# Kernel tuning notes

Measured on AMD Instinct MI355X. Metric: run time of the kernel, lower is better.

## Reference

```python
import jax, jax.numpy as jnp
import numpy as np

D = 1024      # input_dim
H = 16        # num_heads
DH = D // H   # head dim
HID = 4 * D   # SwiGLU hidden
WIN = 128
B, S = 2, 1024


def setup_inputs() -> dict:
    key = jax.random.key(0)
    ks = jax.random.split(key, 16)
    n = lambda k, sh, sc=0.02: jax.random.normal(k, sh, dtype=jnp.float32) * sc
    inp = {
        "fusion": jax.random.normal(ks[0], (B, S, D), dtype=jnp.float32),
        "visual": jax.random.normal(ks[1], (B, S, D), dtype=jnp.float32),
        "text": jax.random.normal(ks[2], (B, S, D), dtype=jnp.float32),
        "audio": jax.random.normal(ks[3], (B, S, D), dtype=jnp.float32),
        "ln1_g": jnp.ones((D,), jnp.float32),
        "ln1_b": jnp.zeros((D,), jnp.float32),
        "Wqkv": n(ks[4], (D, 3 * D)),
        "bqkv": jnp.zeros((3 * D,), jnp.float32),
        "Wo": n(ks[5], (D, D)),
        "bo": jnp.zeros((D,), jnp.float32),
        "ln2_g": jnp.ones((D,), jnp.float32),
        "ln2_b": jnp.zeros((D,), jnp.float32),
        "W1": n(ks[6], (D, HID)),
        "b1": jnp.zeros((HID,), jnp.float32),
        "W2": n(ks[7], (D, HID)),
        "b2": jnp.zeros((HID,), jnp.float32),
        "W3": n(ks[8], (HID, D)),
        "b3": jnp.zeros((D,), jnp.float32),
    }
    return inp


def _layernorm(x, g, b, eps=1e-5):
    mu = jnp.mean(x, axis=-1, keepdims=True)
    var = jnp.var(x, axis=-1, keepdims=True)
    return (x - mu) * jax.lax.rsqrt(var + eps) * g + b


def _block(x, ln1_g, ln1_b, Wqkv, bqkv, Wo, bo, ln2_g, ln2_b, W1, b1, W2, b2, W3, b3):
    # x: [N, S, D] (N = 4*B streams stacked)
    N, S_, _ = x.shape
    h = _layernorm(x, ln1_g, ln1_b)
    qkv = h @ Wqkv + bqkv                              # [N, S, 3D]
    q, k, v = jnp.split(qkv, 3, axis=-1)
    to_heads = lambda t: t.reshape(N, S_, H, DH).transpose(0, 2, 1, 3)  # [N,H,S,DH]
    q, k, v = to_heads(q), to_heads(k), to_heads(v)
    scores = jnp.einsum("nhqd,nhkd->nhqk", q, k) / np.sqrt(DH)
    i = jnp.arange(S_)
    band = jnp.abs(i[:, None] - i[None, :]) <= WIN     # [S, S] local window mask
    scores = jnp.where(band, scores, -jnp.inf)
    probs = jax.nn.softmax(scores, axis=-1)
    ctx = jnp.einsum("nhqk,nhkd->nhqd", probs, v)      # [N,H,S,DH]
    ctx = ctx.transpose(0, 2, 1, 3).reshape(N, S_, D)
    x = x + (ctx @ Wo + bo)
    h2 = _layernorm(x, ln2_g, ln2_b)
    ffn = (jax.nn.silu(h2 @ W1 + b1) * (h2 @ W2 + b2)) @ W3 + b3
    return x + ffn


def reference(fusion, visual, text, audio, ln1_g, ln1_b, Wqkv, bqkv, Wo, bo,
              ln2_g, ln2_b, W1, b1, W2, b2, W3, b3):
    # Same layer applied to each modality -> stack and run once.
    x = jnp.concatenate([fusion, visual, text, audio], axis=0)  # [4B, S, D]
    y = _block(x, ln1_g, ln1_b, Wqkv, bqkv, Wo, bo, ln2_g, ln2_b,
               W1, b1, W2, b2, W3, b3)
    f, vi, t, a = jnp.split(y, 4, axis=0)
    return (f, vi, t, a)
```

## Files before the change

### kernel.cpp

```cpp
#include <hip/hip_runtime.h>

#define S_LEN  1024
#define DMODEL 1024
#define NHEAD  16
#define DHEAD  64
#define MROWS  8192
#define HIDDIM 4096
#define WINR   128

typedef __attribute__((ext_vector_type(8))) short bf16x8;
typedef __attribute__((ext_vector_type(4))) float f32x4;

__device__ __forceinline__ float bf2f(unsigned short u){ return __uint_as_float(((unsigned)u) << 16); }
__device__ __forceinline__ unsigned short f2bf(float f){
  unsigned u = __float_as_uint(f);
  u += 0x7FFFu + ((u >> 16) & 1u);
  return (unsigned short)(u >> 16);
}

__device__ __forceinline__ void gload_lds16(const unsigned short* g, unsigned short* l){
  __builtin_amdgcn_global_load_lds((const __attribute__((address_space(1))) unsigned int*)g,
                                   (__attribute__((address_space(3))) unsigned int*)l, 16, 0, 0);
}

__global__ __launch_bounds__(256) void transpose_w(const float* __restrict__ in,
                                                   unsigned short* __restrict__ out,
                                                   int R, int C){
  __shared__ float tile[32][33];
  const int c0 = blockIdx.x * 32;
  const int r0 = blockIdx.y * 32;
  const int tx = threadIdx.x & 31;
  const int ty = threadIdx.x >> 5;
  #pragma unroll
  for (int i = 0; i < 32; i += 8)
    tile[ty + i][tx] = in[(size_t)(r0 + ty + i) * C + c0 + tx];
  __syncthreads();
  #pragma unroll
  for (int i = 0; i < 32; i += 8)
    out[(size_t)(c0 + ty + i) * R + r0 + tx] = f2bf(tile[tx][ty + i]);
}

__global__ __launch_bounds__(256) void ln_kernel(const float* __restrict__ s0, const float* __restrict__ s1,
                                                 const float* __restrict__ s2, const float* __restrict__ s3,
                                                 const float* __restrict__ g, const float* __restrict__ b,
                                                 unsigned short* __restrict__ out){
  const int row = blockIdx.x;
  const int t = threadIdx.x;
  const float* src = (row < 2048) ? s0 : (row < 4096) ? s1 : (row < 6144) ? s2 : s3;
  const float* x = src + (size_t)(row & 2047) * DMODEL;
  float4 v = *(const float4*)&x[t * 4];
  float sum  = v.x + v.y + v.z + v.w;
  float ssum = v.x*v.x + v.y*v.y + v.z*v.z + v.w*v.w;
  #pragma unroll
  for (int o = 32; o > 0; o >>= 1){
    sum  += __shfl_down(sum, o);
    ssum += __shfl_down(ssum, o);
  }
  __shared__ float red[8];
  if ((t & 63) == 0){ red[t >> 6] = sum; red[4 + (t >> 6)] = ssum; }
  __syncthreads();
  sum  = red[0] + red[1] + red[2] + red[3];
  ssum = red[4] + red[5] + red[6] + red[7];
  const float mu  = sum * (1.f / DMODEL);
  const float var = ssum * (1.f / DMODEL) - mu * mu;
  const float rs  = rsqrtf(var + 1e-5f);
  float4 gg = *(const float4*)&g[t * 4];
  float4 bb = *(const float4*)&b[t * 4];
  ushort4 o;
  o.x = f2bf((v.x - mu) * rs * gg.x + bb.x);
  o.y = f2bf((v.y - mu) * rs * gg.y + bb.y);
  o.z = f2bf((v.z - mu) * rs * gg.z + bb.z);
  o.w = f2bf((v.w - mu) * rs * gg.w + bb.w);
  *(ushort4*)&out[(size_t)row * DMODEL + t * 4] = o;
}

__global__ __launch_bounds__(256) void attn_kernel(const unsigned short* __restrict__ qh,
                                                   const unsigned short* __restrict__ kh,
                                                   const unsigned short* __restrict__ vt,
                                                   unsigned short* __restrict__ ctx){
  __shared__ unsigned short Ks[64 * 64];
  __shared__ unsigned short Vs[64 * 64];
  __shared__ unsigned short Ps[4][16 * 64];
  const int bx = blockIdx.x;
  const int qt = bx & 15, hd = (bx >> 4) & 15, n = bx >> 8;
  const int q0 = qt * 64;
  const int tid = threadIdx.x, lane = tid & 63, w = tid >> 6;
  const int hi = lane >> 4, lo = lane & 15;
  const size_t headoff = (size_t)(n * NHEAD + hd) * S_LEN * DHEAD;
  const unsigned short* kb = kh + headoff;
  const unsigned short* vb = vt + headoff;

  const int qg = q0 + w * 16 + lo;
  bf16x8 bq0 = *(const bf16x8*)(qh + headoff + (size_t)qg * DHEAD + hi * 8);
  bf16x8 bq1 = *(const bf16x8*)(qh + headoff + (size_t)qg * DHEAD + 32 + hi * 8);

  f32x4 oa[4];
  const f32x4 zero = {0.f, 0.f, 0.f, 0.f};
  #pragma unroll
  for (int dj = 0; dj < 4; dj++) oa[dj] = zero;
  float m = -20.f, lsum = 0.f;

  int t_first = q0 - WINR; if (t_first < 0) t_first = 0;
  int t_last  = q0 + 63 + WINR; if (t_last > S_LEN - 1) t_last = S_LEN - 1;

  const int sk = ((lane & 7) ^ (lane >> 3)) * 8;
  const int px = (lo & 7) * 8;

  for (int tb = t_first; tb <= t_last; tb += 64){
    __syncthreads();
    #pragma unroll
    for (int p = 0; p < 2; p++){
      const int r = w * 16 + p * 8 + (lane >> 3);
      gload_lds16(kb + (size_t)(tb + r) * DHEAD + sk, Ks + (w * 16 + p * 8) * 64);
      gload_lds16(vb + (size_t)r * S_LEN + tb + sk, Vs + (w * 16 + p * 8) * 64);
    }
    __syncthreads();

    f32x4 sc[4];
    #pragma unroll
    for (int j = 0; j < 4; j++){
      const int row = j * 16 + lo;
      bf16x8 ak0 = *(const bf16x8*)&Ks[row * 64 + ((hi * 8) ^ px)];
      bf16x8 ak1 = *(const bf16x8*)&Ks[row * 64 + ((32 + hi * 8) ^ px)];
      sc[j] = __builtin_amdgcn_mfma_f32_16x16x32_bf16(ak0, bq0, zero, 0, 0, 0);
      sc[j] = __builtin_amdgcn_mfma_f32_16x16x32_bf16(ak1, bq1, sc[j], 0, 0, 0);
    }

    float mloc = -1e30f;
    #pragma unroll
    for (int j = 0; j < 4; j++)
      #pragma unroll
      for (int r = 0; r < 4; r++){
        const int key = tb + j * 16 + hi * 4 + r;
        float s = sc[j][r] * 0.125f;
        s = ((unsigned)(key - qg + WINR) <= 2u * WINR) ? s : -1e9f;
        sc[j][r] = s;
        mloc = fmaxf(mloc, s);
      }
    mloc = fmaxf(mloc, __shfl_xor(mloc, 16));
    mloc = fmaxf(mloc, __shfl_xor(mloc, 32));
    const float nm = fmaxf(m, mloc);
    const float scale = __expf(m - nm);
    m = nm;
    float psum = 0.f;
    #pragma unroll
    for (int j = 0; j < 4; j++){
      float p0 = __expf(sc[j][0] - nm), p1 = __expf(sc[j][1] - nm);
      float p2 = __expf(sc[j][2] - nm), p3 = __expf(sc[j][3] - nm);
      psum += (p0 + p1) + (p2 + p3);
      ushort4 pw = { f2bf(p0), f2bf(p1), f2bf(p2), f2bf(p3) };
      *(ushort4*)&Ps[w][lo * 64 + ((hi * 4 + 16 * j) ^ px)] = pw;
    }
    psum += __shfl_xor(psum, 16);
    psum += __shfl_xor(psum, 32);
    lsum = lsum * scale + psum;

    float scr[4];
    #pragma unroll
    for (int r = 0; r < 4; r++) scr[r] = __shfl(scale, (lane & 48) + hi * 4 + r);
    #pragma unroll
    for (int dj = 0; dj < 4; dj++)
      #pragma unroll
      for (int r = 0; r < 4; r++) oa[dj][r] *= scr[r];

    bf16x8 pa0 = *(const bf16x8*)&Ps[w][lo * 64 + ((hi * 8) ^ px)];
    bf16x8 pa1 = *(const bf16x8*)&Ps[w][lo * 64 + ((32 + hi * 8) ^ px)];
    #pragma unroll
    for (int dj = 0; dj < 4; dj++){
      const int dr = dj * 16 + lo;
      bf16x8 bv0 = *(const bf16x8*)&Vs[dr * 64 + ((hi * 8) ^ px)];
      bf16x8 bv1 = *(const bf16x8*)&Vs[dr * 64 + ((32 + hi * 8) ^ px)];
      oa[dj] = __builtin_amdgcn_mfma_f32_16x16x32_bf16(pa0, bv0, oa[dj], 0, 0, 0);
      oa[dj] = __builtin_amdgcn_mfma_f32_16x16x32_bf16(pa1, bv1, oa[dj], 0, 0, 0);
    }
  }

  const float inv = 1.f / lsum;
  float invr[4];
  #pragma unroll
  for (int r = 0; r < 4; r++) invr[r] = __shfl(inv, (lane & 48) + hi * 4 + r);
  #pragma unroll
  for (int dj = 0; dj < 4; dj++)
    #pragma unroll
    for (int r = 0; r < 4; r++){
      const int srow = q0 + w * 16 + hi * 4 + r;
      ctx[((size_t)(n * S_LEN + srow)) * DMODEL + hd * DHEAD + dj * 16 + lo] =
          f2bf(oa[dj][r] * invr[r]);
    }
}

struct GemmP {
  const unsigned short* A;
  const unsigned short* Bt;
  int K;
  int N;
  const float* bias;
  const float* r0; const float* r1; const float* r2; const float* r3;
  unsigned short* oq; unsigned short* ok; unsigned short* ov;
  float* of;
};

template<int MODE>
__global__ __launch_bounds__(512, 2) void gemm_bn128(GemmP p){
  __shared__ unsigned short ldsA[2][256 * 64];
  __shared__ unsigned short ldsB[2][128 * 64];
  const int tid  = threadIdx.x;
  const int lane = tid & 63;
  const int w    = tid >> 6;
  const int lo   = lane & 15, hi = lane >> 4;
  const int l3   = lane >> 3;
  const int sk   = ((lane & 7) ^ l3) * 8;
  const int wm   = (w >> 1) * 64;
  const int wn   = (w & 1) * 64;
  const int K    = p.K;

  const int nwg = gridDim.x;
  const int cpx = nwg >> 3;
  const int bsw = ((int)blockIdx.x & 7) * cpx + ((int)blockIdx.x >> 3);
  const int ntn = p.N >> 7;
  const int m0  = (bsw / ntn) * 256;
  const int n0  = (bsw % ntn) * 128;

  f32x4 acc[4][4];
  const f32x4 zero = {0.f, 0.f, 0.f, 0.f};
  #pragma unroll
  for (int i = 0; i < 4; i++)
    #pragma unroll
    for (int j = 0; j < 4; j++) acc[i][j] = zero;

  auto STAGE = [&](int T){
    const int cur = T & 1;
    const int kb  = T * 64;
    #pragma unroll
    for (int i = 0; i < 4; i++){
      const int r0 = w * 32 + i * 8;
      gload_lds16(p.A + (size_t)(m0 + r0 + l3) * K + kb + sk, &ldsA[cur][r0 * 64]);
    }
    #pragma unroll
    for (int i = 0; i < 2; i++){
      const int r0 = w * 16 + i * 8;
      gload_lds16(p.Bt + (size_t)(n0 + r0 + l3) * K + kb + sk, &ldsB[cur][r0 * 64]);
    }
  };

  STAGE(0);

  const int NT = K >> 6;
  for (int T = 0; T < NT; T++){
    const int cur = T & 1;
    if (T + 1 < NT){
      STAGE(T + 1);
      asm volatile("s_waitcnt vmcnt(6)" ::: "memory");
    } else {
      asm volatile("s_waitcnt vmcnt(0)" ::: "memory");
    }
    __builtin_amdgcn_sched_barrier(0);
    __builtin_amdgcn_s_barrier();
    const unsigned short* As_ = ldsA[cur];
    const unsigned short* Bs_ = ldsB[cur];
    #pragma unroll
    for (int kk = 0; kk < 2; kk++){
      bf16x8 af[4], bfr[4];
      #pragma unroll
      for (int i = 0; i < 4; i++){
        const int R = wm + i * 16 + lo;
        af[i] = *(const bf16x8*)&As_[R * 64 + (((kk * 4 + hi) ^ (R & 7)) * 8)];
      }
      #pragma unroll
      for (int j = 0; j < 4; j++){
        const int R = wn + j * 16 + lo;
        bfr[j] = *(const bf16x8*)&Bs_[R * 64 + (((kk * 4 + hi) ^ (R & 7)) * 8)];
      }
      #pragma unroll
      for (int i = 0; i < 4; i++)
        #pragma unroll
        for (int j = 0; j < 4; j++)
          acc[i][j] = __builtin_amdgcn_mfma_f32_16x16x32_bf16(bfr[j], af[i], acc[i][j], 0, 0, 0);
    }
    __builtin_amdgcn_s_barrier();
  }

  if constexpr (MODE == 1 || MODE == 4){
    const float* rs = p.r0;
    if constexpr (MODE == 1){
      const int rblk = m0 + wm;
      rs = (rblk < 2048) ? p.r0 : (rblk < 4096) ? p.r1 : (rblk < 6144) ? p.r2 : p.r3;
    }
    #pragma unroll
    for (int i = 0; i < 4; i++){
      const int row = m0 + wm + i * 16 + lo;
      #pragma unroll
      for (int j = 0; j < 4; j++){
        const int cb = n0 + wn + j * 16 + hi * 4;
        float4 b4 = *(const float4*)&p.bias[cb];
        float4 r4;
        if constexpr (MODE == 1) r4 = *(const float4*)&rs[(size_t)(row & 2047) * DMODEL + cb];
        else                     r4 = *(const float4*)&rs[(size_t)row * DMODEL + cb];
        float4 v;
        v.x = acc[i][j][0] + b4.x + r4.x;
        v.y = acc[i][j][1] + b4.y + r4.y;
        v.z = acc[i][j][2] + b4.z + r4.z;
        v.w = acc[i][j][3] + b4.w + r4.w;
        *(float4*)&p.of[(size_t)row * DMODEL + cb] = v;
      }
    }
  } else {
    __syncthreads();
    unsigned short* sl = &ldsA[0][0] + w * 4096;
    const int nseq = (m0 + wm) >> 10;
    const int sof  = (m0 + wm) & 1023;
    const bool isV = (n0 >> 10) == 2;
    if (!isV){
      #pragma unroll
      for (int i = 0; i < 4; i++){
        const int row = i * 16 + lo;
        #pragma unroll
        for (int j = 0; j < 4; j++){
          const int c  = j * 16 + hi * 4;
          const int cb = n0 + wn + c;
          float4 b4 = *(const float4*)&p.bias[cb];
          ushort4 o = { f2bf(acc[i][j][0] + b4.x), f2bf(acc[i][j][1] + b4.y),
                        f2bf(acc[i][j][2] + b4.z), f2bf(acc[i][j][3] + b4.w) };
          *(ushort4*)&sl[row * 64 + (((c >> 3) ^ (row & 7)) * 8) + (c & 7)] = o;
        }
      }
      asm volatile("s_waitcnt lgkmcnt(0)" ::: "memory");
      __builtin_amdgcn_sched_barrier(0);
      #pragma unroll
      for (int rep = 0; rep < 8; rep++){
        const int row = rep * 8 + l3;
        const int ch  = lane & 7;
        bf16x8 val = *(const bf16x8*)&sl[row * 64 + ((ch ^ (row & 7)) * 8)];
        const int cg = n0 + wn + ch * 8;
        const int hh = (cg & 1023) >> 6, d0 = cg & 63;
        unsigned short* dst = (cg >> 10) ? p.ok : p.oq;
        *(bf16x8*)&dst[((size_t)((nseq * NHEAD + hh) * S_LEN) + sof + row) * DHEAD + d0] = val;
      }
    } else {
      #pragma unroll
      for (int i = 0; i < 4; i++){
        const int s = i * 16 + lo;
        #pragma unroll
        for (int j = 0; j < 4; j++){
          const int cb = n0 + wn + j * 16 + hi * 4;
          float4 b4 = *(const float4*)&p.bias[cb];
          #pragma unroll
          for (int r = 0; r < 4; r++){
            const int d = j * 16 + hi * 4 + r;
            const float bv = (r == 0) ? b4.x : (r == 1) ? b4.y : (r == 2) ? b4.z : b4.w;
            sl[d * 64 + (((s >> 3) ^ (d & 7)) * 8) + (s & 7)] = f2bf(acc[i][j][r] + bv);
          }
        }
      }
      asm volatile("s_waitcnt lgkmcnt(0)" ::: "memory");
      __builtin_amdgcn_sched_barrier(0);
      #pragma unroll
      for (int rep = 0; rep < 8; rep++){
        const int d  = rep * 8 + l3;
        const int ch = lane & 7;
        bf16x8 val = *(const bf16x8*)&sl[d * 64 + ((ch ^ (d & 7)) * 8)];
        const int cg = n0 + wn + d;
        const int hh = (cg & 1023) >> 6, dd = cg & 63;
        *(bf16x8*)&p.ov[((size_t)((nseq * NHEAD + hh) * DHEAD) + dd) * S_LEN + sof + ch * 8] = val;
      }
    }
  }
}

__global__ __launch_bounds__(512, 2) void gemm_ffn(const unsigned short* __restrict__ A,
                                                   const unsigned short* __restrict__ B1t,
                                                   const unsigned short* __restrict__ B2t,
                                                   const float* __restrict__ b1,
                                                   const float* __restrict__ b2,
                                                   unsigned short* __restrict__ out){
  __shared__ unsigned short ldsA[2][256 * 64];
  __shared__ unsigned short ldsB[2][2][128 * 64];
  const int tid  = threadIdx.x;
  const int lane = tid & 63;
  const int w    = tid >> 6;
  const int lo   = lane & 15, hi = lane >> 4;
  const int l3   = lane >> 3;
  const int sk   = ((lane & 7) ^ l3) * 8;
  const int wm   = (w >> 1) * 64;
  const int wn   = (w & 1) * 64;
  const int K    = DMODEL;

  const int nwg = gridDim.x;
  const int cpx = nwg >> 3;
  const int bsw = ((int)blockIdx.x & 7) * cpx + ((int)blockIdx.x >> 3);
  const int m0  = (bsw >> 5) * 256;
  const int n0  = (bsw & 31) * 128;

  f32x4 a1[4][4], a2[4][4];
  const f32x4 zero = {0.f, 0.f, 0.f, 0.f};
  #pragma unroll
  for (int i = 0; i < 4; i++)
    #pragma unroll
    for (int j = 0; j < 4; j++){ a1[i][j] = zero; a2[i][j] = zero; }

  auto STAGE = [&](int T){
    const int cur = T & 1;
    const int kb  = T * 64;
    #pragma unroll
    for (int i = 0; i < 4; i++){
      const int r0 = w * 32 + i * 8;
      gload_lds16(A + (size_t)(m0 + r0 + l3) * K + kb + sk, &ldsA[cur][r0 * 64]);
    }
    #pragma unroll
    for (int i = 0; i < 2; i++){
      const int r0 = w * 16 + i * 8;
      gload_lds16(B1t + (size_t)(n0 + r0 + l3) * K + kb + sk, &ldsB[cur][0][r0 * 64]);
      gload_lds16(B2t + (size_t)(n0 + r0 + l3) * K + kb + sk, &ldsB[cur][1][r0 * 64]);
    }
  };

  STAGE(0);

  const int NT = K >> 6;
  for (int T = 0; T < NT; T++){
    const int cur = T & 1;
    if (T + 1 < NT){
      STAGE(T + 1);
      asm volatile("s_waitcnt vmcnt(8)" ::: "memory");
    } else {
      asm volatile("s_waitcnt vmcnt(0)" ::: "memory");
    }
    __builtin_amdgcn_sched_barrier(0);
    __builtin_amdgcn_s_barrier();
    const unsigned short* As_  = ldsA[cur];
    const unsigned short* Bs1_ = ldsB[cur][0];
    const unsigned short* Bs2_ = ldsB[cur][1];
    #pragma unroll
    for (int kk = 0; kk < 2; kk++){
      bf16x8 af[4], bf1[4], bf2[4];
      #pragma unroll
      for (int i = 0; i < 4; i++){
        const int R = wm + i * 16 + lo;
        af[i] = *(const bf16x8*)&As_[R * 64 + (((kk * 4 + hi) ^ (R & 7)) * 8)];
      }
      #pragma unroll
      for (int j = 0; j < 4; j++){
        const int R = wn + j * 16 + lo;
        const int off = R * 64 + (((kk * 4 + hi) ^ (R & 7)) * 8);
        bf1[j] = *(const bf16x8*)&Bs1_[off];
        bf2[j] = *(const bf16x8*)&Bs2_[off];
      }
      #pragma unroll
      for (int i = 0; i < 4; i++)
        #pragma unroll
        for (int j = 0; j < 4; j++){
          a1[i][j] = __builtin_amdgcn_mfma_f32_16x16x32_bf16(bf1[j], af[i], a1[i][j], 0, 0, 0);
          a2[i][j] = __builtin_amdgcn_mfma_f32_16x16x32_bf16(bf2[j], af[i], a2[i][j], 0, 0, 0);
        }
    }
    __builtin_amdgcn_s_barrier();
  }

  __syncthreads();
  unsigned short* sl = &ldsA[0][0] + w * 4096;
  #pragma unroll
  for (int i = 0; i < 4; i++){
    const int row = i * 16 + lo;
    #pragma unroll
    for (int j = 0; j < 4; j++){
      const int c  = j * 16 + hi * 4;
      const int cb = n0 + wn + c;
      float4 g1 = *(const float4*)&b1[cb];
      float4 g2 = *(const float4*)&b2[cb];
      float v1[4] = { a1[i][j][0] + g1.x, a1[i][j][1] + g1.y, a1[i][j][2] + g1.z, a1[i][j][3] + g1.w };
      float v2[4] = { a2[i][j][0] + g2.x, a2[i][j][1] + g2.y, a2[i][j][2] + g2.z, a2[i][j][3] + g2.w };
      ushort4 o;
      o.x = f2bf(v1[0] / (1.f + __expf(-v1[0])) * v2[0]);
      o.y = f2bf(v1[1] / (1.f + __expf(-v1[1])) * v2[1]);
      o.z = f2bf(v1[2] / (1.f + __expf(-v1[2])) * v2[2]);
      o.w = f2bf(v1[3] / (1.f + __expf(-v1[3])) * v2[3]);
      *(ushort4*)&sl[row * 64 + (((c >> 3) ^ (row & 7)) * 8) + (c & 7)] = o;
    }
  }
  asm volatile("s_waitcnt lgkmcnt(0)" ::: "memory");
  __builtin_amdgcn_sched_barrier(0);
  #pragma unroll
  for (int rep = 0; rep < 8; rep++){
    const int row = rep * 8 + l3;
    const int ch  = lane & 7;
    bf16x8 val = *(const bf16x8*)&sl[row * 64 + ((ch ^ (row & 7)) * 8)];
    *(bf16x8*)&out[(size_t)(m0 + wm + row) * HIDDIM + n0 + wn + ch * 8] = val;
  }
}

extern "C" void kernel_launch(void* const* d_in, const int* in_sizes, int n_in,
                              void* d_out, int out_size, void* d_ws, size_t ws_size,
                              hipStream_t stream){
  const float* fin  = (const float*)d_in[0];
  const float* vis  = (const float*)d_in[1];
  const float* txt  = (const float*)d_in[2];
  const float* aud  = (const float*)d_in[3];
  const float* ln1g = (const float*)d_in[4];
  const float* ln1b = (const float*)d_in[5];
  const float* Wqkv = (const float*)d_in[6];
  const float* bqkv = (const float*)d_in[7];
  const float* Wo   = (const float*)d_in[8];
  const float* bo   = (const float*)d_in[9];
  const float* ln2g = (const float*)d_in[10];
  const float* ln2b = (const float*)d_in[11];
  const float* W1   = (const float*)d_in[12];
  const float* b1   = (const float*)d_in[13];
  const float* W2   = (const float*)d_in[14];
  const float* b2   = (const float*)d_in[15];
  const float* W3   = (const float*)d_in[16];
  const float* b3   = (const float*)d_in[17];

  char* ws = (char*)d_ws;
  unsigned short* Wqkv_t = (unsigned short*)(ws + 0);
  unsigned short* Wo_t   = (unsigned short*)(ws + 6291456);
  unsigned short* W1t    = (unsigned short*)(ws + 8388608);
  unsigned short* W2t    = (unsigned short*)(ws + 16777216);
  unsigned short* W3t    = (unsigned short*)(ws + 25165824);
  unsigned short* h      = (unsigned short*)(ws + 33554432);
  unsigned short* qh     = (unsigned short*)(ws + 50331648);
  unsigned short* kh     = (unsigned short*)(ws + 67108864);
  unsigned short* vhT    = (unsigned short*)(ws + 83886080);
  unsigned short* ctx    = (unsigned short*)(ws + 100663296);
  float*          x1     = (float*)(ws + 117440512);
  unsigned short* t1     = qh;

  transpose_w<<<dim3(3072/32, 1024/32), 256, 0, stream>>>(Wqkv, Wqkv_t, 1024, 3072);
  transpose_w<<<dim3(1024/32, 1024/32), 256, 0, stream>>>(Wo,   Wo_t,   1024, 1024);
  transpose_w<<<dim3(4096/32, 1024/32), 256, 0, stream>>>(W1,   W1t,    1024, 4096);
  transpose_w<<<dim3(4096/32, 1024/32), 256, 0, stream>>>(W2,   W2t,    1024, 4096);
  transpose_w<<<dim3(1024/32, 4096/32), 256, 0, stream>>>(W3,   W3t,    4096, 1024);

  ln_kernel<<<MROWS, 256, 0, stream>>>(fin, vis, txt, aud, ln1g, ln1b, h);

  {
    GemmP p{};
    p.A = h; p.Bt = Wqkv_t; p.K = 1024; p.N = 3072; p.bias = bqkv;
    p.oq = qh; p.ok = kh; p.ov = vhT;
    gemm_bn128<0><<<768, 512, 0, stream>>>(p);
  }

  attn_kernel<<<2048, 256, 0, stream>>>(qh, kh, vhT, ctx);

  {
    GemmP p{};
    p.A = ctx; p.Bt = Wo_t; p.K = 1024; p.N = 1024; p.bias = bo;
    p.r0 = fin; p.r1 = vis; p.r2 = txt; p.r3 = aud;
    p.of = x1;
    gemm_bn128<1><<<256, 512, 0, stream>>>(p);
  }

  ln_kernel<<<MROWS, 256, 0, stream>>>(x1, x1 + (size_t)2048 * 1024, x1 + (size_t)4096 * 1024,
                                       x1 + (size_t)6144 * 1024, ln2g, ln2b, h);

  gemm_ffn<<<1024, 512, 0, stream>>>(h, W1t, W2t, b1, b2, t1);

  {
    GemmP p{};
    p.A = t1; p.Bt = W3t; p.K = HIDDIM; p.N = 1024; p.bias = b3;
    p.r0 = x1;
    p.of = (float*)d_out;
    gemm_bn128<4><<<256, 512, 0, stream>>>(p);
  }

  (void)in_sizes; (void)n_in; (void)out_size; (void)ws_size;
}
```

Measured before the change: 402.9 us.

## Split FFN gate/up GEMM into two phases with staggered A/B prefetch

Restructures the dual-B SwiGLU GEMM main loop into two half-phases: the first computes the W1 product while prefetching the next A tile, and the second computes the W2 product while prefetching the next B1/B2 tiles. Loads are issued after the barrier, with finer-grained vmcnt waits, so global-to-LDS traffic overlaps MFMA work more evenly. It also uses s_setprio around the MFMA blocks and fewer live B fragments to cut register pressure. The cost is an extra barrier per K step and A fragments being re-read from LDS twice.

```diff
diff --git a/kernel.cpp b/kernel.cpp
--- a/kernel.cpp
+++ b/kernel.cpp
@@ -374,7 +374,8 @@
                                                    const float* __restrict__ b2,
                                                    unsigned short* __restrict__ out){
   __shared__ unsigned short ldsA[2][256 * 64];
-  __shared__ unsigned short ldsB[2][2][128 * 64];
+  __shared__ unsigned short ldsB1[2][128 * 64];
+  __shared__ unsigned short ldsB2[2][128 * 64];
   const int tid  = threadIdx.x;
   const int lane = tid & 63;
   const int w    = tid >> 6;
@@ -383,7 +384,6 @@
   const int sk   = ((lane & 7) ^ l3) * 8;
   const int wm   = (w >> 1) * 64;
   const int wn   = (w & 1) * 64;
-  const int K    = DMODEL;
 
   const int nwg = gridDim.x;
   const int cpx = nwg >> 3;
@@ -398,41 +398,48 @@
     #pragma unroll
     for (int j = 0; j < 4; j++){ a1[i][j] = zero; a2[i][j] = zero; }
 
-  auto STAGE = [&](int T){
+  auto STAGE_A = [&](int T){
     const int cur = T & 1;
     const int kb  = T * 64;
     #pragma unroll
-    for (int i = 0; i < 4; i++){
-      const int r0 = w * 32 + i * 8;
-      gload_lds16(A + (size_t)(m0 + r0 + l3) * K + kb + sk, &ldsA[cur][r0 * 64]);
-    }
-    #pragma unroll
-    for (int i = 0; i < 2; i++){
-      const int r0 = w * 16 + i * 8;
-      gload_lds16(B1t + (size_t)(n0 + r0 + l3) * K + kb + sk, &ldsB[cur][0][r0 * 64]);
-      gload_lds16(B2t + (size_t)(n0 + r0 + l3) * K + kb + sk, &ldsB[cur][1][r0 * 64]);
+    for (int c = 0; c < 4; c++){
+      const int r0 = c * 64 + w * 8;
+      gload_lds16(A + (size_t)(m0 + r0 + l3) * DMODEL + kb + sk, &ldsA[cur][r0 * 64]);
     }
   };
-
-  STAGE(0);
-
-  const int NT = K >> 6;
+  auto STAGE_B = [&](int T){
+    const int cur = T & 1;
+    const int kb  = T * 64;
+    #pragma unroll
+    for (int h = 0; h < 2; h++){
+      const int r0 = h * 64 + w * 8;
+      gload_lds16(B1t + (size_t)(n0 + r0 + l3) * DMODEL + kb + sk, &ldsB1[cur][r0 * 64]);
+    }
+    #pragma unroll
+    for (int h = 0; h < 2; h++){
+      const int r0 = h * 64 + w * 8;
+      gload_lds16(B2t + (size_t)(n0 + r0 + l3) * DMODEL + kb + sk, &ldsB2[cur][r0 * 64]);
+    }
+  };
+
+  STAGE_A(0);
+  STAGE_B(0);
+
+  const int NT = DMODEL >> 6;
   for (int T = 0; T < NT; T++){
     const int cur = T & 1;
-    if (T + 1 < NT){
-      STAGE(T + 1);
-      asm volatile("s_waitcnt vmcnt(8)" ::: "memory");
-    } else {
-      asm volatile("s_waitcnt vmcnt(0)" ::: "memory");
-    }
+    const unsigned short* As_  = ldsA[cur];
+    const unsigned short* Bs1_ = ldsB1[cur];
+    const unsigned short* Bs2_ = ldsB2[cur];
+
+    asm volatile("s_waitcnt vmcnt(2)" ::: "memory");
     __builtin_amdgcn_sched_barrier(0);
     __builtin_amdgcn_s_barrier();
-    const unsigned short* As_  = ldsA[cur];
-    const unsigned short* Bs1_ = ldsB[cur][0];
-    const unsigned short* Bs2_ = ldsB[cur][1];
+
+    if (T + 1 < NT) STAGE_A(T + 1);
     #pragma unroll
     for (int kk = 0; kk < 2; kk++){
-      bf16x8 af[4], bf1[4], bf2[4];
+      bf16x8 af[4], bfr[4];
       #pragma unroll
       for (int i = 0; i < 4; i++){
         const int R = wm + i * 16 + lo;
@@ -441,19 +448,44 @@
       #pragma unroll
       for (int j = 0; j < 4; j++){
         const int R = wn + j * 16 + lo;
-        const int off = R * 64 + (((kk * 4 + hi) ^ (R & 7)) * 8);
-        bf1[j] = *(const bf16x8*)&Bs1_[off];
-        bf2[j] = *(const bf16x8*)&Bs2_[off];
-      }
+        bfr[j] = *(const bf16x8*)&Bs1_[R * 64 + (((kk * 4 + hi) ^ (R & 7)) * 8)];
+      }
+      __builtin_amdgcn_s_setprio(1);
       #pragma unroll
       for (int i = 0; i < 4; i++)
         #pragma unroll
-        for (int j = 0; j < 4; j++){
-          a1[i][j] = __builtin_amdgcn_mfma_f32_16x16x32_bf16(bf1[j], af[i], a1[i][j], 0, 0, 0);
-          a2[i][j] = __builtin_amdgcn_mfma_f32_16x16x32_bf16(bf2[j], af[i], a2[i][j], 0, 0, 0);
-        }
-    }
+        for (int j = 0; j < 4; j++)
+          a1[i][j] = __builtin_amdgcn_mfma_f32_16x16x32_bf16(bfr[j], af[i], a1[i][j], 0, 0, 0);
+      __builtin_amdgcn_s_setprio(0);
+    }
+
+    if (T + 1 < NT) asm volatile("s_waitcnt vmcnt(4)" ::: "memory");
+    else            asm volatile("s_waitcnt vmcnt(0)" ::: "memory");
+    __builtin_amdgcn_sched_barrier(0);
     __builtin_amdgcn_s_barrier();
+
+    if (T + 1 < NT) STAGE_B(T + 1);
+    #pragma unroll
+    for (int kk = 0; kk < 2; kk++){
+      bf16x8 af[4], bfr[4];
+      #pragma unroll
+      for (int i = 0; i < 4; i++){
+        const int R = wm + i * 16 + lo;
+        af[i] = *(const bf16x8*)&As_[R * 64 + (((kk * 4 + hi) ^ (R & 7)) * 8)];
+      }
+      #pragma unroll
+      for (int j = 0; j < 4; j++){
+        const int R = wn + j * 16 + lo;
+        bfr[j] = *(const bf16x8*)&Bs2_[R * 64 + (((kk * 4 + hi) ^ (R & 7)) * 8)];
+      }
+      __builtin_amdgcn_s_setprio(1);
+      #pragma unroll
+      for (int i = 0; i < 4; i++)
+        #pragma unroll
+        for (int j = 0; j < 4; j++)
+          a2[i][j] = __builtin_amdgcn_mfma_f32_16x16x32_bf16(bfr[j], af[i], a2[i][j], 0, 0, 0);
+      __builtin_amdgcn_s_setprio(0);
+    }
   }
 
   __syncthreads();
```

Measured after the change: 442.9 us. +9.9%, slower.

## Shrink GEMM tiles to 128x128 with 256 threads and drop FFN double buffering

Applied to the files above, without the earlier changes.

Every GEMM now uses a 128x128 output tile computed by 4 waves (256 threads) instead of 256x128 with 8 waves, and grid sizes are doubled to match. The FFN GEMM also drops its double-buffered async LDS pipeline in favour of a single buffer guarded by two __syncthreads per K step, which cuts LDS use per block. Smaller tiles and less LDS should let more blocks fit on each CU, but each block reuses its loaded data less, and the FFN kernel no longer overlaps global loads with MFMA work. The epilogue still indexes LDS with w*4096 on the now smaller ldsA, which relies on the buffers lying next to each other and could be unsafe.

```diff
diff --git a/kernel.cpp b/kernel.cpp
--- a/kernel.cpp
+++ b/kernel.cpp
@@ -201,8 +201,8 @@
 };
 
 template<int MODE>
-__global__ __launch_bounds__(512, 2) void gemm_bn128(GemmP p){
-  __shared__ unsigned short ldsA[2][256 * 64];
+__global__ __launch_bounds__(256, 2) void gemm_bn128(GemmP p){
+  __shared__ unsigned short ldsA[2][128 * 64];
   __shared__ unsigned short ldsB[2][128 * 64];
   const int tid  = threadIdx.x;
   const int lane = tid & 63;
@@ -218,7 +218,7 @@
   const int cpx = nwg >> 3;
   const int bsw = ((int)blockIdx.x & 7) * cpx + ((int)blockIdx.x >> 3);
   const int ntn = p.N >> 7;
-  const int m0  = (bsw / ntn) * 256;
+  const int m0  = (bsw / ntn) * 128;
   const int n0  = (bsw % ntn) * 128;
 
   f32x4 acc[4][4];
@@ -232,13 +232,13 @@
     const int cur = T & 1;
     const int kb  = T * 64;
     #pragma unroll
-    for (int i = 0; i < 4; i++){
-      const int r0 = w * 32 + i * 8;
+    for (int c = 0; c < 4; c++){
+      const int r0 = w * 32 + c * 8;
       gload_lds16(p.A + (size_t)(m0 + r0 + l3) * K + kb + sk, &ldsA[cur][r0 * 64]);
     }
     #pragma unroll
-    for (int i = 0; i < 2; i++){
-      const int r0 = w * 16 + i * 8;
+    for (int c = 0; c < 4; c++){
+      const int r0 = w * 32 + c * 8;
       gload_lds16(p.Bt + (size_t)(n0 + r0 + l3) * K + kb + sk, &ldsB[cur][r0 * 64]);
     }
   };
@@ -250,7 +250,7 @@
     const int cur = T & 1;
     if (T + 1 < NT){
       STAGE(T + 1);
-      asm volatile("s_waitcnt vmcnt(6)" ::: "memory");
+      asm volatile("s_waitcnt vmcnt(8)" ::: "memory");
     } else {
       asm volatile("s_waitcnt vmcnt(0)" ::: "memory");
     }
@@ -367,14 +367,15 @@
   }
 }
 
-__global__ __launch_bounds__(512, 2) void gemm_ffn(const unsigned short* __restrict__ A,
+__global__ __launch_bounds__(256, 2) void gemm_ffn(const unsigned short* __restrict__ A,
                                                    const unsigned short* __restrict__ B1t,
                                                    const unsigned short* __restrict__ B2t,
                                                    const float* __restrict__ b1,
                                                    const float* __restrict__ b2,
                                                    unsigned short* __restrict__ out){
-  __shared__ unsigned short ldsA[2][256 * 64];
-  __shared__ unsigned short ldsB[2][2][128 * 64];
+  __shared__ unsigned short ldsA[128 * 64];
+  __shared__ unsigned short ldsB1[128 * 64];
+  __shared__ unsigned short ldsB2[128 * 64];
   const int tid  = threadIdx.x;
   const int lane = tid & 63;
   const int w    = tid >> 6;
@@ -383,12 +384,11 @@
   const int sk   = ((lane & 7) ^ l3) * 8;
   const int wm   = (w >> 1) * 64;
   const int wn   = (w & 1) * 64;
-  const int K    = DMODEL;
 
   const int nwg = gridDim.x;
   const int cpx = nwg >> 3;
   const int bsw = ((int)blockIdx.x & 7) * cpx + ((int)blockIdx.x >> 3);
-  const int m0  = (bsw >> 5) * 256;
+  const int m0  = (bsw >> 5) * 128;
   const int n0  = (bsw & 31) * 128;
 
   f32x4 a1[4][4], a2[4][4];
@@ -398,52 +398,33 @@
     #pragma unroll
     for (int j = 0; j < 4; j++){ a1[i][j] = zero; a2[i][j] = zero; }
 
-  auto STAGE = [&](int T){
-    const int cur = T & 1;
-    const int kb  = T * 64;
-    #pragma unroll
-    for (int i = 0; i < 4; i++){
-      const int r0 = w * 32 + i * 8;
-      gload_lds16(A + (size_t)(m0 + r0 + l3) * K + kb + sk, &ldsA[cur][r0 * 64]);
-    }
-    #pragma unroll
-    for (int i = 0; i < 2; i++){
-      const int r0 = w * 16 + i * 8;
-      gload_lds16(B1t + (size_t)(n0 + r0 + l3) * K + kb + sk, &ldsB[cur][0][r0 * 64]);
-      gload_lds16(B2t + (size_t)(n0 + r0 + l3) * K + kb + sk, &ldsB[cur][1][r0 * 64]);
-    }
-  };
-
-  STAGE(0);
-
-  const int NT = K >> 6;
+  const int NT = DMODEL >> 6;
   for (int T = 0; T < NT; T++){
-    const int cur = T & 1;
-    if (T + 1 < NT){
-      STAGE(T + 1);
-      asm volatile("s_waitcnt vmcnt(8)" ::: "memory");
-    } else {
-      asm volatile("s_waitcnt vmcnt(0)" ::: "memory");
-    }
-    __builtin_amdgcn_sched_barrier(0);
-    __builtin_amdgcn_s_barrier();
-    const unsigned short* As_  = ldsA[cur];
-    const unsigned short* Bs1_ = ldsB[cur][0];
-    const unsigned short* Bs2_ = ldsB[cur][1];
+    const int kb = T * 64;
+    __syncthreads();
+    #pragma unroll
+    for (int c = 0; c < 4; c++){
+      const int r0 = w * 32 + c * 8;
+      gload_lds16(A   + (size_t)(m0 + r0 + l3) * DMODEL + kb + sk, &ldsA[r0 * 64]);
+      gload_lds16(B1t + (size_t)(n0 + r0 + l3) * DMODEL + kb + sk, &ldsB1[r0 * 64]);
+      gload_lds16(B2t + (size_t)(n0 + r0 + l3) * DMODEL + kb + sk, &ldsB2[r0 * 64]);
+    }
+    __syncthreads();
+
     #pragma unroll
     for (int kk = 0; kk < 2; kk++){
       bf16x8 af[4], bf1[4], bf2[4];
       #pragma unroll
       for (int i = 0; i < 4; i++){
         const int R = wm + i * 16 + lo;
-        af[i] = *(const bf16x8*)&As_[R * 64 + (((kk * 4 + hi) ^ (R & 7)) * 8)];
+        af[i] = *(const bf16x8*)&ldsA[R * 64 + (((kk * 4 + hi) ^ (R & 7)) * 8)];
       }
       #pragma unroll
       for (int j = 0; j < 4; j++){
         const int R = wn + j * 16 + lo;
         const int off = R * 64 + (((kk * 4 + hi) ^ (R & 7)) * 8);
-        bf1[j] = *(const bf16x8*)&Bs1_[off];
-        bf2[j] = *(const bf16x8*)&Bs2_[off];
+        bf1[j] = *(const bf16x8*)&ldsB1[off];
+        bf2[j] = *(const bf16x8*)&ldsB2[off];
       }
       #pragma unroll
       for (int i = 0; i < 4; i++)
@@ -453,11 +434,10 @@
           a2[i][j] = __builtin_amdgcn_mfma_f32_16x16x32_bf16(bf2[j], af[i], a2[i][j], 0, 0, 0);
         }
     }
-    __builtin_amdgcn_s_barrier();
   }
 
   __syncthreads();
-  unsigned short* sl = &ldsA[0][0] + w * 4096;
+  unsigned short* sl = &ldsA[0] + w * 4096;
   #pragma unroll
   for (int i = 0; i < 4; i++){
     const int row = i * 16 + lo;
@@ -536,7 +516,7 @@
     GemmP p{};
     p.A = h; p.Bt = Wqkv_t; p.K = 1024; p.N = 3072; p.bias = bqkv;
     p.oq = qh; p.ok = kh; p.ov = vhT;
-    gemm_bn128<0><<<768, 512, 0, stream>>>(p);
+    gemm_bn128<0><<<1536, 256, 0, stream>>>(p);
   }
 
   attn_kernel<<<2048, 256, 0, stream>>>(qh, kh, vhT, ctx);
@@ -546,20 +526,20 @@
     p.A = ctx; p.Bt = Wo_t; p.K = 1024; p.N = 1024; p.bias = bo;
     p.r0 = fin; p.r1 = vis; p.r2 = txt; p.r3 = aud;
     p.of = x1;
-    gemm_bn128<1><<<256, 512, 0, stream>>>(p);
+    gemm_bn128<1><<<512, 256, 0, stream>>>(p);
   }
 
   ln_kernel<<<MROWS, 256, 0, stream>>>(x1, x1 + (size_t)2048 * 1024, x1 + (size_t)4096 * 1024,
                                        x1 + (size_t)6144 * 1024, ln2g, ln2b, h);
 
-  gemm_ffn<<<1024, 512, 0, stream>>>(h, W1t, W2t, b1, b2, t1);
+  gemm_ffn<<<2048, 256, 0, stream>>>(h, W1t, W2t, b1, b2, t1);
 
   {
     GemmP p{};
     p.A = t1; p.Bt = W3t; p.K = HIDDIM; p.N = 1024; p.bias = b3;
     p.r0 = x1;
     p.of = (float*)d_out;
-    gemm_bn128<4><<<256, 512, 0, stream>>>(p);
+    gemm_bn128<4><<<512, 256, 0, stream>>>(p);
   }
 
   (void)in_sizes; (void)n_in; (void)out_size; (void)ws_size;
```

Measured after the change: 389.1 us. 3.4% less time.
